# Kernel optimization log

Measured on AMD Instinct MI355X. Metric: run time of the kernel, lower is better.

Reference implementation:

```python
import jax, jax.numpy as jnp
import numpy as np

N_NODES = 50000
N_EDGES = 800000
F_IN = 128
HEADS = 4
C_OUT = 16
NEG_SLOPE = 0.2


def setup_inputs() -> dict:
    key = jax.random.key(0)
    k1, k2, k3, k4, k5 = jax.random.split(key, 5)
    x = jax.random.normal(k1, (N_NODES, F_IN), dtype=jnp.float32)
    edge_index = jax.random.randint(k2, (2, N_EDGES), 0, N_NODES, dtype=jnp.int64)
    W = jax.random.normal(k3, (F_IN, HEADS * C_OUT), dtype=jnp.float32) * (1.0 / np.sqrt(F_IN))
    att_src = jax.random.normal(k4, (HEADS, C_OUT), dtype=jnp.float32) * (1.0 / np.sqrt(C_OUT))
    att_dst = jax.random.normal(k5, (HEADS, C_OUT), dtype=jnp.float32) * (1.0 / np.sqrt(C_OUT))
    bias = jnp.zeros((HEADS * C_OUT,), dtype=jnp.float32)
    return {"x": x, "edge_index": edge_index, "W": W,
            "att_src": att_src, "att_dst": att_dst, "bias": bias}


def reference(x, edge_index, W, att_src, att_dst, bias):
    N = x.shape[0]
    H, C = att_src.shape
    # PyG GATConv default: add self-loops
    loop = jnp.arange(N, dtype=edge_index.dtype)
    ei = jnp.concatenate([edge_index, jnp.stack([loop, loop])], axis=1)  # [2, E+N]
    src, dst = ei[0], ei[1]

    h = (x @ W).reshape(N, H, C)                      # [N, H, C]
    a_src = jnp.einsum('nhc,hc->nh', h, att_src)      # [N, H]
    a_dst = jnp.einsum('nhc,hc->nh', h, att_dst)      # [N, H]

    e = a_src[src] + a_dst[dst]                       # [E+N, H]
    e = jnp.where(e > 0, e, NEG_SLOPE * e)            # leaky_relu(0.2)

    # segment softmax over destination node (every segment has a self-loop)
    m = jax.ops.segment_max(e, dst, num_segments=N)   # [N, H]
    e = jnp.exp(e - m[dst])
    s = jax.ops.segment_sum(e, dst, num_segments=N)   # [N, H]
    alpha = e / (s[dst] + 1e-16)                      # [E+N, H]

    # scatter-aggregate weighted neighbor features
    out = jax.ops.segment_sum(h[src] * alpha[..., None], dst, num_segments=N)  # [N, H, C]
    out = out.reshape(N, H * C) + bias                # concat heads + bias
    return out, alpha
```

## Files before the change

### kernel.cpp

```cpp
#include <hip/hip_runtime.h>

#define N_NODES 50000
#define N_EDGES 800000
#define EN      (N_EDGES + N_NODES)
#define F_IN    128
#define HC      64
#define NEG_SLOPE 0.2f
#define NBUCK   196
#define BCAP    5120
#define P3_EPB  4096
#define LIN_BLOCKS 782
#define NBLK    196
#define RCAP    64
#define NSLOT   (NBLK * RCAP)
#define XPAD    136

typedef __attribute__((ext_vector_type(8))) short bf16x8;
typedef __attribute__((ext_vector_type(4))) float f32x4;

static __device__ __forceinline__ unsigned short f2bf(float f) {
    unsigned int b = __float_as_uint(f);
    return (unsigned short)((b + 0x7FFFu + ((b >> 16) & 1u)) >> 16);
}

__global__ __launch_bounds__(256) void
kA_linear_bin(const float* __restrict__ x, const float* __restrict__ W,
              const float* __restrict__ att_src, const float* __restrict__ att_dst,
              const int* __restrict__ ei,
              unsigned short* __restrict__ hbf, float* __restrict__ a_src,
              float* __restrict__ a_dst, int* __restrict__ bins,
              int* __restrict__ cntg) {
    __shared__ unsigned short xs[64][XPAD];
    __shared__ unsigned short wt[80][XPAD];
    __shared__ int bcnt_l[NBUCK];
    const int tid = threadIdx.x;

    if (blockIdx.x >= LIN_BLOCKS) {
        const int blk = blockIdx.x - LIN_BLOCKS;
        for (int i = tid; i < NBUCK; i += 256) bcnt_l[i] = 0;
        __syncthreads();
        const int base = blk * P3_EPB;
        #pragma unroll
        for (int j = 0; j < 16; ++j) {
            int i = base + j * 256 + tid;
            if (i < N_EDGES) {
                int sv = ei[i];
                int d  = ei[N_EDGES + i];
                int bk = d >> 8;
                int r  = atomicAdd(&bcnt_l[bk], 1);
                if (r < RCAP)
                    bins[(bk * NBLK + blk) * RCAP + r] = sv | ((d & 255) << 16);
            }
        }
        __syncthreads();
        for (int b = tid; b < NBUCK; b += 256)
            cntg[b * NBLK + blk] = min(bcnt_l[b], RCAP);
        return;
    }

    const int wv   = tid >> 6;
    const int l    = tid & 63;
    const int base = blockIdx.x * 64;
    const int c16  = l & 15;
    const int grp  = l >> 4;

    #pragma unroll
    for (int it = 0; it < 8; ++it) {
        int f  = it * 1024 + tid * 4;
        int k  = f >> 6;
        int cl = f & 63;
        float4 v = *(const float4*)(W + (size_t)k * HC + cl);
        wt[cl + 0][k] = f2bf(v.x);
        wt[cl + 1][k] = f2bf(v.y);
        wt[cl + 2][k] = f2bf(v.z);
        wt[cl + 3][k] = f2bf(v.w);
    }

    #pragma unroll
    for (int it = 0; it < 8; ++it) {
        int f   = it * 1024 + tid * 4;
        int row = f >> 7, k = f & 127;
        int gr  = base + row;
        float4 v = {0.f, 0.f, 0.f, 0.f};
        if (gr < N_NODES) v = *(const float4*)(x + (size_t)gr * F_IN + k);
        ushort4 u = {f2bf(v.x), f2bf(v.y), f2bf(v.z), f2bf(v.w)};
        *(ushort4*)(&xs[row][k]) = u;
    }

    {
        const int wk = tid >> 1;
        const int wo = (tid & 1) * 4;
        const float* wrow = W + (size_t)wk * HC;
        #pragma unroll
        for (int oo = 0; oo < 4; ++oo) {
            const int o = wo + oo;
            const int h = o & 3;
            const float* av = (o < 4) ? (att_src + h * 16) : (att_dst + h * 16);
            float a = 0.f;
            #pragma unroll
            for (int c = 0; c < 16; c += 4) {
                float4 w4 = *(const float4*)(wrow + h * 16 + c);
                float4 a4 = *(const float4*)(av + c);
                a += w4.x * a4.x + w4.y * a4.y + w4.z * a4.z + w4.w * a4.w;
            }
            wt[64 + o][wk] = f2bf(a);
        }
    }
    __syncthreads();

    bf16x8 Bf[5][4];
    #pragma unroll
    for (int t = 0; t < 5; ++t)
        #pragma unroll
        for (int kk = 0; kk < 4; ++kk)
            Bf[t][kk] = *(const bf16x8*)(&wt[t * 16 + c16][kk * 32 + grp * 8]);

    const int r0 = wv * 16;
    f32x4 C[4], C4;
    #pragma unroll
    for (int t = 0; t < 4; ++t) C[t] = (f32x4){0.f, 0.f, 0.f, 0.f};
    C4 = (f32x4){0.f, 0.f, 0.f, 0.f};
    bf16x8 A[4];
    #pragma unroll
    for (int kk = 0; kk < 4; ++kk)
        A[kk] = *(const bf16x8*)(&xs[r0 + c16][kk * 32 + grp * 8]);
    #pragma unroll
    for (int t = 0; t < 4; ++t)
        #pragma unroll
        for (int kk = 0; kk < 4; ++kk)
            C[t] = __builtin_amdgcn_mfma_f32_16x16x32_bf16(A[kk], Bf[t][kk], C[t], 0, 0, 0);
    #pragma unroll
    for (int kk = 0; kk < 4; ++kk)
        C4 = __builtin_amdgcn_mfma_f32_16x16x32_bf16(A[kk], Bf[4][kk], C4, 0, 0, 0);

    #pragma unroll
    for (int j = 0; j < 4; ++j) {
        const int row = base + r0 + grp * 4 + j;
        if (row < N_NODES) {
            #pragma unroll
            for (int t = 0; t < 4; ++t)
                hbf[(size_t)row * HC + t * 16 + c16] = f2bf(C[t][j]);
            if (c16 < 4)      a_src[row * 4 + c16]       = C4[j];
            else if (c16 < 8) a_dst[row * 4 + (c16 - 4)] = C4[j];
        }
    }
}

__global__ __launch_bounds__(256) void
p4_csr(const int* __restrict__ bins, const int* __restrict__ cntg,
       int* __restrict__ row_info, int* __restrict__ srcs) {
    __shared__ int psum[256];
    __shared__ int cnt[256], sm[256], cur[256];
    const int b = blockIdx.x, tid = threadIdx.x;
    const int node = (b << 8) + tid;

    psum[tid] = (tid < NBLK) ? cntg[b * NBLK + tid] : 0;
    cnt[tid] = (node < N_NODES) ? 1 : 0;
    __syncthreads();
    for (int off = 1; off < 256; off <<= 1) {
        int t = (tid >= off) ? psum[tid - off] : 0;
        __syncthreads();
        psum[tid] += t;
        __syncthreads();
    }
    const int T = psum[255];
    const int* bb = bins + (size_t)b * NSLOT;

    int pvs[20];
    #pragma unroll
    for (int it = 0; it < 20; ++it) {
        const int i = tid + it * 256;
        if (i < T) {
            int lo = 0, hi = NBLK - 1;
            while (lo < hi) { int mid = (lo + hi) >> 1;
                              if (psum[mid] > i) hi = mid; else lo = mid + 1; }
            const int k  = i - (lo ? psum[lo - 1] : 0);
            const int pv = bb[lo * RCAP + k];
            pvs[it] = pv;
            atomicAdd(&cnt[pv >> 16], 1);
        }
    }
    __syncthreads();

    int v = cnt[tid];
    sm[tid] = v;
    __syncthreads();
    for (int off = 1; off < 256; off <<= 1) {
        int t = (tid >= off) ? sm[tid - off] : 0;
        __syncthreads();
        sm[tid] += t;
        __syncthreads();
    }
    const int ex = sm[tid] - v;
    const int sbase = b * BCAP;

    if (node < N_NODES) {
        row_info[node] = ((sbase + ex) << 8) | v;
        srcs[sbase + ex] = node;
    }
    cur[tid] = ex + 1;
    __syncthreads();
    #pragma unroll
    for (int it = 0; it < 20; ++it) {
        const int i = tid + it * 256;
        if (i < T) {
            const int pv = pvs[it];
            const int p  = atomicAdd(&cur[pv >> 16], 1);
            srcs[sbase + p] = pv & 0xFFFF;
        }
    }
}

__global__ __launch_bounds__(256) void
k_agg(const int* __restrict__ row_info, const int* __restrict__ srcs,
      const float* __restrict__ a_src, const float* __restrict__ a_dst,
      const unsigned int* __restrict__ hw,
      const float* __restrict__ bias, float* __restrict__ out,
      float* __restrict__ s_inv) {
    __shared__ int   s_lds[4][4][16];
    __shared__ float p_lds[4][4][16][4];

    const int tid  = threadIdx.x;
    const int wv   = tid >> 6;
    const int lane = tid & 63;
    const int g    = lane >> 4;
    const int l    = lane & 15;
    const int hd   = l >> 2;
    const int d    = blockIdx.x * 16 + wv * 4 + g;

    const int info   = row_info[d];
    const int begin  = info >> 8;
    const int cnt    = info & 255;
    const int nchunk = (cnt + 15) >> 4;
    const float4 ad  = *(const float4*)(a_dst + d * 4);

    float4 ps = {0.f, 0.f, 0.f, 0.f};
    float a0 = 0.f, a1 = 0.f, a2 = 0.f, a3 = 0.f;

    for (int c = 0; c < nchunk; ++c) {
        const int k0 = begin + c * 16;
        const int m  = min(16, begin + cnt - k0);
        const int s = srcs[k0 + (l < m ? l : m - 1)];
        float4 p = {0.f, 0.f, 0.f, 0.f};
        if (l < m) {
            float4 as = *(const float4*)(a_src + s * 4);
            float e0 = as.x + ad.x, e1 = as.y + ad.y, e2 = as.z + ad.z, e3 = as.w + ad.w;
            e0 = e0 > 0.f ? e0 : NEG_SLOPE * e0;
            e1 = e1 > 0.f ? e1 : NEG_SLOPE * e1;
            e2 = e2 > 0.f ? e2 : NEG_SLOPE * e2;
            e3 = e3 > 0.f ? e3 : NEG_SLOPE * e3;
            p.x = __expf(e0); p.y = __expf(e1); p.z = __expf(e2); p.w = __expf(e3);
            ps.x += p.x; ps.y += p.y; ps.z += p.z; ps.w += p.w;
        }
        s_lds[wv][g][l] = s;
        *(float4*)(&p_lds[wv][g][l][0]) = p;
        __threadfence_block();

        const int mp = (m + 3) & ~3;
        for (int e = 0; e < mp; e += 4) {
            int s0 = s_lds[wv][g][e + 0], s1 = s_lds[wv][g][e + 1];
            int s2 = s_lds[wv][g][e + 2], s3 = s_lds[wv][g][e + 3];
            float p0 = p_lds[wv][g][e + 0][hd], p1 = p_lds[wv][g][e + 1][hd];
            float p2 = p_lds[wv][g][e + 2][hd], p3 = p_lds[wv][g][e + 3][hd];
            uint2 u0 = *(const uint2*)(hw + (size_t)s0 * 32 + l * 2);
            uint2 u1 = *(const uint2*)(hw + (size_t)s1 * 32 + l * 2);
            uint2 u2 = *(const uint2*)(hw + (size_t)s2 * 32 + l * 2);
            uint2 u3 = *(const uint2*)(hw + (size_t)s3 * 32 + l * 2);
            a0 += __uint_as_float(u0.x << 16)         * p0;
            a1 += __uint_as_float(u0.x & 0xFFFF0000u) * p0;
            a2 += __uint_as_float(u0.y << 16)         * p0;
            a3 += __uint_as_float(u0.y & 0xFFFF0000u) * p0;
            a0 += __uint_as_float(u1.x << 16)         * p1;
            a1 += __uint_as_float(u1.x & 0xFFFF0000u) * p1;
            a2 += __uint_as_float(u1.y << 16)         * p1;
            a3 += __uint_as_float(u1.y & 0xFFFF0000u) * p1;
            a0 += __uint_as_float(u2.x << 16)         * p2;
            a1 += __uint_as_float(u2.x & 0xFFFF0000u) * p2;
            a2 += __uint_as_float(u2.y << 16)         * p2;
            a3 += __uint_as_float(u2.y & 0xFFFF0000u) * p2;
            a0 += __uint_as_float(u3.x << 16)         * p3;
            a1 += __uint_as_float(u3.x & 0xFFFF0000u) * p3;
            a2 += __uint_as_float(u3.y << 16)         * p3;
            a3 += __uint_as_float(u3.y & 0xFFFF0000u) * p3;
        }
        __threadfence_block();
    }

    #pragma unroll
    for (int mm = 1; mm < 16; mm <<= 1) {
        ps.x += __shfl_xor(ps.x, mm);
        ps.y += __shfl_xor(ps.y, mm);
        ps.z += __shfl_xor(ps.z, mm);
        ps.w += __shfl_xor(ps.w, mm);
    }
    const float4 inv = {1.f / (ps.x + 1e-16f), 1.f / (ps.y + 1e-16f),
                        1.f / (ps.z + 1e-16f), 1.f / (ps.w + 1e-16f)};
    if (l == 0) *(float4*)(s_inv + d * 4) = inv;

    const float invh = (hd == 0) ? inv.x : (hd == 1) ? inv.y : (hd == 2) ? inv.z : inv.w;
    float4 o;
    o.x = a0 * invh + bias[l * 4 + 0];
    o.y = a1 * invh + bias[l * 4 + 1];
    o.z = a2 * invh + bias[l * 4 + 2];
    o.w = a3 * invh + bias[l * 4 + 3];
    *(float4*)(out + (size_t)d * HC + l * 4) = o;
}

__global__ void k_alpha(const int* __restrict__ ei, const float* __restrict__ a_src,
                        const float* __restrict__ a_dst, const float* __restrict__ s_inv,
                        float* __restrict__ alpha_out) {
    int i2 = blockIdx.x * 256 + threadIdx.x;
    if (i2 >= EN / 2) return;
    const int i = i2 * 2;
    int s0, s1, d0, d1;
    if (i < N_EDGES) {
        int2 sp = *(const int2*)(ei + i);
        int2 dp = *(const int2*)(ei + N_EDGES + i);
        s0 = sp.x; s1 = sp.y; d0 = dp.x; d1 = dp.y;
    } else {
        s0 = d0 = i - N_EDGES;
        s1 = d1 = i + 1 - N_EDGES;
    }

    float4 as0 = *(const float4*)(a_src + s0 * 4);
    float4 ad0 = *(const float4*)(a_dst + d0 * 4);
    float4 iv0 = *(const float4*)(s_inv + d0 * 4);
    float4 as1 = *(const float4*)(a_src + s1 * 4);
    float4 ad1 = *(const float4*)(a_dst + d1 * 4);
    float4 iv1 = *(const float4*)(s_inv + d1 * 4);

    float e0, e1, e2, e3;
    e0 = as0.x + ad0.x; e1 = as0.y + ad0.y; e2 = as0.z + ad0.z; e3 = as0.w + ad0.w;
    e0 = e0 > 0.f ? e0 : NEG_SLOPE * e0;
    e1 = e1 > 0.f ? e1 : NEG_SLOPE * e1;
    e2 = e2 > 0.f ? e2 : NEG_SLOPE * e2;
    e3 = e3 > 0.f ? e3 : NEG_SLOPE * e3;
    float4 al0 = {__expf(e0) * iv0.x, __expf(e1) * iv0.y,
                  __expf(e2) * iv0.z, __expf(e3) * iv0.w};
    e0 = as1.x + ad1.x; e1 = as1.y + ad1.y; e2 = as1.z + ad1.z; e3 = as1.w + ad1.w;
    e0 = e0 > 0.f ? e0 : NEG_SLOPE * e0;
    e1 = e1 > 0.f ? e1 : NEG_SLOPE * e1;
    e2 = e2 > 0.f ? e2 : NEG_SLOPE * e2;
    e3 = e3 > 0.f ? e3 : NEG_SLOPE * e3;
    float4 al1 = {__expf(e0) * iv1.x, __expf(e1) * iv1.y,
                  __expf(e2) * iv1.z, __expf(e3) * iv1.w};

    *(float4*)(alpha_out + (size_t)i * 4)     = al0;
    *(float4*)(alpha_out + (size_t)i * 4 + 4) = al1;
}

extern "C" void kernel_launch(void* const* d_in, const int* in_sizes, int n_in,
                              void* d_out, int out_size, void* d_ws, size_t ws_size,
                              hipStream_t stream) {
    const float* x       = (const float*)d_in[0];
    const int*   ei      = (const int*)d_in[1];
    const float* W       = (const float*)d_in[2];
    const float* att_src = (const float*)d_in[3];
    const float* att_dst = (const float*)d_in[4];
    const float* bias    = (const float*)d_in[5];

    float* out       = (float*)d_out;
    float* alpha_out = (float*)d_out + (size_t)N_NODES * HC;

    char* ws = (char*)d_ws;
    size_t off = 0;
    unsigned short* hbf = (unsigned short*)(ws + off); off += (size_t)N_NODES * HC * 2;
    float* a_src   = (float*)(ws + off); off += (size_t)N_NODES * 4 * 4;
    float* a_dst   = (float*)(ws + off); off += (size_t)N_NODES * 4 * 4;
    float* s_inv   = (float*)(ws + off); off += (size_t)N_NODES * 4 * 4;
    int* row_info  = (int*)(ws + off);   off += (size_t)N_NODES * 4;
    int* srcs      = (int*)(ws + off);   off += (size_t)NBUCK * BCAP * 4;
    int* bins      = (int*)(ws + off);   off += (size_t)NBUCK * NSLOT * 4;
    int* cntg      = (int*)(ws + off);   off += (size_t)NBUCK * NBLK * 4;

    kA_linear_bin<<<LIN_BLOCKS + NBLK, 256, 0, stream>>>(x, W, att_src, att_dst, ei,
                                                         hbf, a_src, a_dst, bins, cntg);
    p4_csr<<<NBUCK, 256, 0, stream>>>(bins, cntg, row_info, srcs);
    k_agg<<<N_NODES / 16, 256, 0, stream>>>(row_info, srcs, a_src, a_dst,
                                            (const unsigned int*)hbf, bias, out, s_inv);
    k_alpha<<<(EN / 2 + 255) / 256, 256, 0, stream>>>(ei, a_src, a_dst, s_inv, alpha_out);
}
```

Baseline: 80.93 us.

## Replace two-level bucket binning with global degree count, scan, and atomic scatter CSR

Edges are no longer binned into per-block, per-bucket slots and then compacted. The new path counts in-degrees with global atomics alongside the linear layer, runs a per-bucket exclusive scan to get row offsets, and places sources with a separate atomic-cursor scatter kernel. This drops the bins and count buffers and the binary-search compaction, and removes the old per-bin RCAP cap that could silently drop edges. In exchange it adds a memset, an extra kernel launch and heavy global atomic traffic on random destinations, and the order of neighbours within a row is now nondeterministic.

```diff
diff --git a/kernel.cpp b/kernel.cpp
--- a/kernel.cpp
+++ b/kernel.cpp
@@ -10,9 +10,7 @@
 #define BCAP    5120
 #define P3_EPB  4096
 #define LIN_BLOCKS 782
-#define NBLK    196
-#define RCAP    64
-#define NSLOT   (NBLK * RCAP)
+#define NCNT    196
 #define XPAD    136
 
 typedef __attribute__((ext_vector_type(8))) short bf16x8;
@@ -24,37 +22,22 @@
 }
 
 __global__ __launch_bounds__(256) void
-kA_linear_bin(const float* __restrict__ x, const float* __restrict__ W,
+kA_linear_cnt(const float* __restrict__ x, const float* __restrict__ W,
               const float* __restrict__ att_src, const float* __restrict__ att_dst,
               const int* __restrict__ ei,
               unsigned short* __restrict__ hbf, float* __restrict__ a_src,
-              float* __restrict__ a_dst, int* __restrict__ bins,
-              int* __restrict__ cntg) {
+              float* __restrict__ a_dst, int* __restrict__ deg) {
     __shared__ unsigned short xs[64][XPAD];
     __shared__ unsigned short wt[80][XPAD];
-    __shared__ int bcnt_l[NBUCK];
     const int tid = threadIdx.x;
 
     if (blockIdx.x >= LIN_BLOCKS) {
-        const int blk = blockIdx.x - LIN_BLOCKS;
-        for (int i = tid; i < NBUCK; i += 256) bcnt_l[i] = 0;
-        __syncthreads();
-        const int base = blk * P3_EPB;
+        const int base = (blockIdx.x - LIN_BLOCKS) * P3_EPB;
         #pragma unroll
         for (int j = 0; j < 16; ++j) {
             int i = base + j * 256 + tid;
-            if (i < N_EDGES) {
-                int sv = ei[i];
-                int d  = ei[N_EDGES + i];
-                int bk = d >> 8;
-                int r  = atomicAdd(&bcnt_l[bk], 1);
-                if (r < RCAP)
-                    bins[(bk * NBLK + blk) * RCAP + r] = sv | ((d & 255) << 16);
-            }
-        }
-        __syncthreads();
-        for (int b = tid; b < NBUCK; b += 256)
-            cntg[b * NBLK + blk] = min(bcnt_l[b], RCAP);
+            if (i < N_EDGES) atomicAdd(&deg[ei[N_EDGES + i]], 1);
+        }
         return;
     }
 
@@ -147,42 +130,13 @@
 }
 
 __global__ __launch_bounds__(256) void
-p4_csr(const int* __restrict__ bins, const int* __restrict__ cntg,
-       int* __restrict__ row_info, int* __restrict__ srcs) {
-    __shared__ int psum[256];
-    __shared__ int cnt[256], sm[256], cur[256];
+k_scan(const int* __restrict__ deg, int* __restrict__ row_info,
+       int* __restrict__ srcs, int* __restrict__ cur) {
+    __shared__ int sm[256];
     const int b = blockIdx.x, tid = threadIdx.x;
     const int node = (b << 8) + tid;
 
-    psum[tid] = (tid < NBLK) ? cntg[b * NBLK + tid] : 0;
-    cnt[tid] = (node < N_NODES) ? 1 : 0;
-    __syncthreads();
-    for (int off = 1; off < 256; off <<= 1) {
-        int t = (tid >= off) ? psum[tid - off] : 0;
-        __syncthreads();
-        psum[tid] += t;
-        __syncthreads();
-    }
-    const int T = psum[255];
-    const int* bb = bins + (size_t)b * NSLOT;
-
-    int pvs[20];
-    #pragma unroll
-    for (int it = 0; it < 20; ++it) {
-        const int i = tid + it * 256;
-        if (i < T) {
-            int lo = 0, hi = NBLK - 1;
-            while (lo < hi) { int mid = (lo + hi) >> 1;
-                              if (psum[mid] > i) hi = mid; else lo = mid + 1; }
-            const int k  = i - (lo ? psum[lo - 1] : 0);
-            const int pv = bb[lo * RCAP + k];
-            pvs[it] = pv;
-            atomicAdd(&cnt[pv >> 16], 1);
-        }
-    }
-    __syncthreads();
-
-    int v = cnt[tid];
+    const int v = (node < N_NODES) ? deg[node] + 1 : 0;
     sm[tid] = v;
     __syncthreads();
     for (int off = 1; off < 256; off <<= 1) {
@@ -191,24 +145,25 @@
         sm[tid] += t;
         __syncthreads();
     }
-    const int ex = sm[tid] - v;
-    const int sbase = b * BCAP;
-
+    const int begin = b * BCAP + (sm[tid] - v);
     if (node < N_NODES) {
-        row_info[node] = ((sbase + ex) << 8) | v;
-        srcs[sbase + ex] = node;
-    }
-    cur[tid] = ex + 1;
-    __syncthreads();
-    #pragma unroll
-    for (int it = 0; it < 20; ++it) {
-        const int i = tid + it * 256;
-        if (i < T) {
-            const int pv = pvs[it];
-            const int p  = atomicAdd(&cur[pv >> 16], 1);
-            srcs[sbase + p] = pv & 0xFFFF;
-        }
-    }
+        row_info[node] = (begin << 8) | v;
+        srcs[begin]    = node;
+        cur[node]      = begin + 1;
+    }
+}
+
+__global__ __launch_bounds__(256) void
+k_scatter(const int* __restrict__ ei, int* __restrict__ cur, int* __restrict__ srcs) {
+    const int t0 = (blockIdx.x * 256 + threadIdx.x) * 4;
+    if (t0 >= N_EDGES) return;
+    int4 sp = *(const int4*)(ei + t0);
+    int4 dp = *(const int4*)(ei + N_EDGES + t0);
+    int p;
+    p = atomicAdd(&cur[dp.x], 1); srcs[p] = sp.x;
+    p = atomicAdd(&cur[dp.y], 1); srcs[p] = sp.y;
+    p = atomicAdd(&cur[dp.z], 1); srcs[p] = sp.z;
+    p = atomicAdd(&cur[dp.w], 1); srcs[p] = sp.w;
 }
 
 __global__ __launch_bounds__(256) void
@@ -370,12 +325,14 @@
     float* s_inv   = (float*)(ws + off); off += (size_t)N_NODES * 4 * 4;
     int* row_info  = (int*)(ws + off);   off += (size_t)N_NODES * 4;
     int* srcs      = (int*)(ws + off);   off += (size_t)NBUCK * BCAP * 4;
-    int* bins      = (int*)(ws + off);   off += (size_t)NBUCK * NSLOT * 4;
-    int* cntg      = (int*)(ws + off);   off += (size_t)NBUCK * NBLK * 4;
-
-    kA_linear_bin<<<LIN_BLOCKS + NBLK, 256, 0, stream>>>(x, W, att_src, att_dst, ei,
-                                                         hbf, a_src, a_dst, bins, cntg);
-    p4_csr<<<NBUCK, 256, 0, stream>>>(bins, cntg, row_info, srcs);
+    int* deg       = (int*)(ws + off);   off += (size_t)N_NODES * 4;
+    int* cur       = (int*)(ws + off);   off += (size_t)N_NODES * 4;
+
+    hipMemsetAsync(deg, 0, (size_t)N_NODES * 4, stream);
+    kA_linear_cnt<<<LIN_BLOCKS + NCNT, 256, 0, stream>>>(x, W, att_src, att_dst, ei,
+                                                         hbf, a_src, a_dst, deg);
+    k_scan<<<NBUCK, 256, 0, stream>>>(deg, row_info, srcs, cur);
+    k_scatter<<<(N_EDGES / 4 + 255) / 256, 256, 0, stream>>>(ei, cur, srcs);
     k_agg<<<N_NODES / 16, 256, 0, stream>>>(row_info, srcs, a_src, a_dst,
                                             (const unsigned int*)hbf, bias, out, s_inv);
     k_alpha<<<(EN / 2 + 255) / 256, 256, 0, stream>>>(ei, a_src, a_dst, s_inv, alpha_out);
```

New measurement: 135.2 us. 1.67x slower.

## Split bf16 feature table into two halves and aggregate in two passes

Applied to the files above, without the earlier changes.

The bf16 projected features are stored as two separate 32-channel tables (heads 0-1 and heads 2-3). Aggregation runs twice, once per half, so each pass gathers from a 3.2 MB table that fits better in cache. The first pass computes the softmax denominators and the second reads them back. Nontemporal loads and stores are added for srcs, out and alpha. The cost is that the CSR traversal, the a_src gathers and the exp work are repeated across two launches.

```diff
diff --git a/kernel.cpp b/kernel.cpp
--- a/kernel.cpp
+++ b/kernel.cpp
@@ -17,6 +17,7 @@
 
 typedef __attribute__((ext_vector_type(8))) short bf16x8;
 typedef __attribute__((ext_vector_type(4))) float f32x4;
+typedef __attribute__((ext_vector_type(2))) float f32x2;
 
 static __device__ __forceinline__ unsigned short f2bf(float f) {
     unsigned int b = __float_as_uint(f);
@@ -27,9 +28,9 @@
 kA_linear_bin(const float* __restrict__ x, const float* __restrict__ W,
               const float* __restrict__ att_src, const float* __restrict__ att_dst,
               const int* __restrict__ ei,
-              unsigned short* __restrict__ hbf, float* __restrict__ a_src,
-              float* __restrict__ a_dst, int* __restrict__ bins,
-              int* __restrict__ cntg) {
+              unsigned short* __restrict__ hbfA, unsigned short* __restrict__ hbfB,
+              float* __restrict__ a_src, float* __restrict__ a_dst,
+              int* __restrict__ bins, int* __restrict__ cntg) {
     __shared__ unsigned short xs[64][XPAD];
     __shared__ unsigned short wt[80][XPAD];
     __shared__ int bcnt_l[NBUCK];
@@ -137,9 +138,10 @@
     for (int j = 0; j < 4; ++j) {
         const int row = base + r0 + grp * 4 + j;
         if (row < N_NODES) {
-            #pragma unroll
-            for (int t = 0; t < 4; ++t)
-                hbf[(size_t)row * HC + t * 16 + c16] = f2bf(C[t][j]);
+            hbfA[(size_t)row * 32 +  0 + c16] = f2bf(C[0][j]);
+            hbfA[(size_t)row * 32 + 16 + c16] = f2bf(C[1][j]);
+            hbfB[(size_t)row * 32 +  0 + c16] = f2bf(C[2][j]);
+            hbfB[(size_t)row * 32 + 16 + c16] = f2bf(C[3][j]);
             if (c16 < 4)      a_src[row * 4 + c16]       = C4[j];
             else if (c16 < 8) a_dst[row * 4 + (c16 - 4)] = C4[j];
         }
@@ -212,20 +214,20 @@
 }
 
 __global__ __launch_bounds__(256) void
-k_agg(const int* __restrict__ row_info, const int* __restrict__ srcs,
-      const float* __restrict__ a_src, const float* __restrict__ a_dst,
-      const unsigned int* __restrict__ hw,
-      const float* __restrict__ bias, float* __restrict__ out,
-      float* __restrict__ s_inv) {
+k_agg2(const int* __restrict__ row_info, const int* __restrict__ srcs,
+       const float* __restrict__ a_src, const float* __restrict__ a_dst,
+       const unsigned int* __restrict__ hwh,
+       const float* __restrict__ bias, float* __restrict__ out,
+       float* __restrict__ s_inv, const int half) {
     __shared__ int   s_lds[4][4][16];
-    __shared__ float p_lds[4][4][16][4];
+    __shared__ float p_lds[4][4][16][2];
 
     const int tid  = threadIdx.x;
     const int wv   = tid >> 6;
     const int lane = tid & 63;
     const int g    = lane >> 4;
     const int l    = lane & 15;
-    const int hd   = l >> 2;
+    const int hd2  = l >> 3;
     const int d    = blockIdx.x * 16 + wv * 4 + g;
 
     const int info   = row_info[d];
@@ -235,13 +237,13 @@
     const float4 ad  = *(const float4*)(a_dst + d * 4);
 
     float4 ps = {0.f, 0.f, 0.f, 0.f};
-    float a0 = 0.f, a1 = 0.f, a2 = 0.f, a3 = 0.f;
+    float a0 = 0.f, a1 = 0.f;
 
     for (int c = 0; c < nchunk; ++c) {
         const int k0 = begin + c * 16;
         const int m  = min(16, begin + cnt - k0);
-        const int s = srcs[k0 + (l < m ? l : m - 1)];
-        float4 p = {0.f, 0.f, 0.f, 0.f};
+        const int s = __builtin_nontemporal_load(srcs + k0 + (l < m ? l : m - 1));
+        float2 pst = {0.f, 0.f};
         if (l < m) {
             float4 as = *(const float4*)(a_src + s * 4);
             float e0 = as.x + ad.x, e1 = as.y + ad.y, e2 = as.z + ad.z, e3 = as.w + ad.w;
@@ -249,61 +251,64 @@
             e1 = e1 > 0.f ? e1 : NEG_SLOPE * e1;
             e2 = e2 > 0.f ? e2 : NEG_SLOPE * e2;
             e3 = e3 > 0.f ? e3 : NEG_SLOPE * e3;
-            p.x = __expf(e0); p.y = __expf(e1); p.z = __expf(e2); p.w = __expf(e3);
-            ps.x += p.x; ps.y += p.y; ps.z += p.z; ps.w += p.w;
+            if (half == 0) {
+                float p0 = __expf(e0), p1 = __expf(e1);
+                float p2 = __expf(e2), p3 = __expf(e3);
+                ps.x += p0; ps.y += p1; ps.z += p2; ps.w += p3;
+                pst.x = p0; pst.y = p1;
+            } else {
+                pst.x = __expf(e2); pst.y = __expf(e3);
+            }
         }
         s_lds[wv][g][l] = s;
-        *(float4*)(&p_lds[wv][g][l][0]) = p;
+        *(float2*)(&p_lds[wv][g][l][0]) = pst;
         __threadfence_block();
 
         const int mp = (m + 3) & ~3;
         for (int e = 0; e < mp; e += 4) {
             int s0 = s_lds[wv][g][e + 0], s1 = s_lds[wv][g][e + 1];
             int s2 = s_lds[wv][g][e + 2], s3 = s_lds[wv][g][e + 3];
-            float p0 = p_lds[wv][g][e + 0][hd], p1 = p_lds[wv][g][e + 1][hd];
-            float p2 = p_lds[wv][g][e + 2][hd], p3 = p_lds[wv][g][e + 3][hd];
-            uint2 u0 = *(const uint2*)(hw + (size_t)s0 * 32 + l * 2);
-            uint2 u1 = *(const uint2*)(hw + (size_t)s1 * 32 + l * 2);
-            uint2 u2 = *(const uint2*)(hw + (size_t)s2 * 32 + l * 2);
-            uint2 u3 = *(const uint2*)(hw + (size_t)s3 * 32 + l * 2);
-            a0 += __uint_as_float(u0.x << 16)         * p0;
-            a1 += __uint_as_float(u0.x & 0xFFFF0000u) * p0;
-            a2 += __uint_as_float(u0.y << 16)         * p0;
-            a3 += __uint_as_float(u0.y & 0xFFFF0000u) * p0;
-            a0 += __uint_as_float(u1.x << 16)         * p1;
-            a1 += __uint_as_float(u1.x & 0xFFFF0000u) * p1;
-            a2 += __uint_as_float(u1.y << 16)         * p1;
-            a3 += __uint_as_float(u1.y & 0xFFFF0000u) * p1;
-            a0 += __uint_as_float(u2.x << 16)         * p2;
-            a1 += __uint_as_float(u2.x & 0xFFFF0000u) * p2;
-            a2 += __uint_as_float(u2.y << 16)         * p2;
-            a3 += __uint_as_float(u2.y & 0xFFFF0000u) * p2;
-            a0 += __uint_as_float(u3.x << 16)         * p3;
-            a1 += __uint_as_float(u3.x & 0xFFFF0000u) * p3;
-            a2 += __uint_as_float(u3.y << 16)         * p3;
-            a3 += __uint_as_float(u3.y & 0xFFFF0000u) * p3;
+            float p0 = p_lds[wv][g][e + 0][hd2], p1 = p_lds[wv][g][e + 1][hd2];
+            float p2 = p_lds[wv][g][e + 2][hd2], p3 = p_lds[wv][g][e + 3][hd2];
+            unsigned int u0 = hwh[(size_t)s0 * 16 + l];
+            unsigned int u1 = hwh[(size_t)s1 * 16 + l];
+            unsigned int u2 = hwh[(size_t)s2 * 16 + l];
+            unsigned int u3 = hwh[(size_t)s3 * 16 + l];
+            a0 += __uint_as_float(u0 << 16)         * p0;
+            a1 += __uint_as_float(u0 & 0xFFFF0000u) * p0;
+            a0 += __uint_as_float(u1 << 16)         * p1;
+            a1 += __uint_as_float(u1 & 0xFFFF0000u) * p1;
+            a0 += __uint_as_float(u2 << 16)         * p2;
+            a1 += __uint_as_float(u2 & 0xFFFF0000u) * p2;
+            a0 += __uint_as_float(u3 << 16)         * p3;
+            a1 += __uint_as_float(u3 & 0xFFFF0000u) * p3;
         }
         __threadfence_block();
     }
 
-    #pragma unroll
-    for (int mm = 1; mm < 16; mm <<= 1) {
-        ps.x += __shfl_xor(ps.x, mm);
-        ps.y += __shfl_xor(ps.y, mm);
-        ps.z += __shfl_xor(ps.z, mm);
-        ps.w += __shfl_xor(ps.w, mm);
-    }
-    const float4 inv = {1.f / (ps.x + 1e-16f), 1.f / (ps.y + 1e-16f),
-                        1.f / (ps.z + 1e-16f), 1.f / (ps.w + 1e-16f)};
-    if (l == 0) *(float4*)(s_inv + d * 4) = inv;
-
-    const float invh = (hd == 0) ? inv.x : (hd == 1) ? inv.y : (hd == 2) ? inv.z : inv.w;
-    float4 o;
-    o.x = a0 * invh + bias[l * 4 + 0];
-    o.y = a1 * invh + bias[l * 4 + 1];
-    o.z = a2 * invh + bias[l * 4 + 2];
-    o.w = a3 * invh + bias[l * 4 + 3];
-    *(float4*)(out + (size_t)d * HC + l * 4) = o;
+    float invl;
+    if (half == 0) {
+        #pragma unroll
+        for (int mm = 1; mm < 16; mm <<= 1) {
+            ps.x += __shfl_xor(ps.x, mm);
+            ps.y += __shfl_xor(ps.y, mm);
+            ps.z += __shfl_xor(ps.z, mm);
+            ps.w += __shfl_xor(ps.w, mm);
+        }
+        const float4 inv = {1.f / (ps.x + 1e-16f), 1.f / (ps.y + 1e-16f),
+                            1.f / (ps.z + 1e-16f), 1.f / (ps.w + 1e-16f)};
+        if (l == 0) *(float4*)(s_inv + d * 4) = inv;
+        invl = hd2 ? inv.y : inv.x;
+    } else {
+        const float2 iv = *(const float2*)(s_inv + d * 4 + 2);
+        invl = hd2 ? iv.y : iv.x;
+    }
+
+    const int ch = half * 32 + l * 2;
+    f32x2 o;
+    o.x = a0 * invl + bias[ch + 0];
+    o.y = a1 * invl + bias[ch + 1];
+    __builtin_nontemporal_store(o, (f32x2*)(out + (size_t)d * HC + ch));
 }
 
 __global__ void k_alpha(const int* __restrict__ ei, const float* __restrict__ a_src,
@@ -335,18 +340,18 @@
     e1 = e1 > 0.f ? e1 : NEG_SLOPE * e1;
     e2 = e2 > 0.f ? e2 : NEG_SLOPE * e2;
     e3 = e3 > 0.f ? e3 : NEG_SLOPE * e3;
-    float4 al0 = {__expf(e0) * iv0.x, __expf(e1) * iv0.y,
-                  __expf(e2) * iv0.z, __expf(e3) * iv0.w};
+    f32x4 al0 = {__expf(e0) * iv0.x, __expf(e1) * iv0.y,
+                 __expf(e2) * iv0.z, __expf(e3) * iv0.w};
     e0 = as1.x + ad1.x; e1 = as1.y + ad1.y; e2 = as1.z + ad1.z; e3 = as1.w + ad1.w;
     e0 = e0 > 0.f ? e0 : NEG_SLOPE * e0;
     e1 = e1 > 0.f ? e1 : NEG_SLOPE * e1;
     e2 = e2 > 0.f ? e2 : NEG_SLOPE * e2;
     e3 = e3 > 0.f ? e3 : NEG_SLOPE * e3;
-    float4 al1 = {__expf(e0) * iv1.x, __expf(e1) * iv1.y,
-                  __expf(e2) * iv1.z, __expf(e3) * iv1.w};
-
-    *(float4*)(alpha_out + (size_t)i * 4)     = al0;
-    *(float4*)(alpha_out + (size_t)i * 4 + 4) = al1;
+    f32x4 al1 = {__expf(e0) * iv1.x, __expf(e1) * iv1.y,
+                 __expf(e2) * iv1.z, __expf(e3) * iv1.w};
+
+    __builtin_nontemporal_store(al0, (f32x4*)(alpha_out + (size_t)i * 4));
+    __builtin_nontemporal_store(al1, (f32x4*)(alpha_out + (size_t)i * 4 + 4));
 }
 
 extern "C" void kernel_launch(void* const* d_in, const int* in_sizes, int n_in,
@@ -364,7 +369,8 @@
 
     char* ws = (char*)d_ws;
     size_t off = 0;
-    unsigned short* hbf = (unsigned short*)(ws + off); off += (size_t)N_NODES * HC * 2;
+    unsigned short* hbfA = (unsigned short*)(ws + off); off += (size_t)N_NODES * 32 * 2;
+    unsigned short* hbfB = (unsigned short*)(ws + off); off += (size_t)N_NODES * 32 * 2;
     float* a_src   = (float*)(ws + off); off += (size_t)N_NODES * 4 * 4;
     float* a_dst   = (float*)(ws + off); off += (size_t)N_NODES * 4 * 4;
     float* s_inv   = (float*)(ws + off); off += (size_t)N_NODES * 4 * 4;
@@ -374,9 +380,14 @@
     int* cntg      = (int*)(ws + off);   off += (size_t)NBUCK * NBLK * 4;
 
     kA_linear_bin<<<LIN_BLOCKS + NBLK, 256, 0, stream>>>(x, W, att_src, att_dst, ei,
-                                                         hbf, a_src, a_dst, bins, cntg);
+                                                         hbfA, hbfB, a_src, a_dst,
+                                                         bins, cntg);
     p4_csr<<<NBUCK, 256, 0, stream>>>(bins, cntg, row_info, srcs);
-    k_agg<<<N_NODES / 16, 256, 0, stream>>>(row_info, srcs, a_src, a_dst,
-                                            (const unsigned int*)hbf, bias, out, s_inv);
+    k_agg2<<<N_NODES / 16, 256, 0, stream>>>(row_info, srcs, a_src, a_dst,
+                                             (const unsigned int*)hbfA, bias, out,
+                                             s_inv, 0);
+    k_agg2<<<N_NODES / 16, 256, 0, stream>>>(row_info, srcs, a_src, a_dst,
+                                             (const unsigned int*)hbfB, bias, out,
+                                             s_inv, 1);
     k_alpha<<<(EN / 2 + 255) / 256, 256, 0, stream>>>(ei, a_src, a_dst, s_inv, alpha_out);
 }
```

Measured after the change: 100.2 us. 1.24x slower.
